# Optimization experiments

Measured on AMD Instinct MI355X. Metric: run time of the kernel, lower is better.

## Reference

```python
import jax, jax.numpy as jnp
import numpy as np

B, T = 4096, 512          # batch, max seq len
V, E, H, O = 57, 20, 128, 18  # vocab, embed, hidden, classes


def setup_inputs() -> dict:
    key = jax.random.key(0)
    ks = jax.random.split(key, 9)
    x = jax.random.randint(ks[0], (B, T), 0, V)
    lens = jax.random.randint(ks[1], (B,), 1, T + 1)
    x_lengths = jnp.sort(lens)[::-1]  # pack_padded_sequence needs descending lengths
    s = 1.0 / np.sqrt(H)
    emb = jax.random.normal(ks[2], (V, E), dtype=jnp.float32)
    W_ih = jax.random.uniform(ks[3], (H, E), minval=-s, maxval=s, dtype=jnp.float32)
    W_hh = jax.random.uniform(ks[4], (H, H), minval=-s, maxval=s, dtype=jnp.float32)
    b_ih = jax.random.uniform(ks[5], (H,), minval=-s, maxval=s, dtype=jnp.float32)
    b_hh = jax.random.uniform(ks[6], (H,), minval=-s, maxval=s, dtype=jnp.float32)
    so = 1.0 / np.sqrt(H)
    W_out = jax.random.uniform(ks[7], (O, H), minval=-so, maxval=so, dtype=jnp.float32)
    b_out = jax.random.uniform(ks[8], (O,), minval=-so, maxval=so, dtype=jnp.float32)
    return {"x": x, "x_lengths": x_lengths, "emb": emb, "W_ih": W_ih,
            "W_hh": W_hh, "b_ih": b_ih, "b_hh": b_hh, "W_out": W_out, "b_out": b_out}


def reference(x, x_lengths, emb, W_ih, W_hh, b_ih, b_hh, W_out, b_out):
    xe = emb[x]                                            # [B,T,E] embedding gather
    # precompute input projection + both biases once (hoisted out of recurrence)
    xw = jnp.einsum('bte,he->bth', xe, W_ih) + b_ih + b_hh  # [B,T,H]
    valid = jnp.arange(T)[None, :] < x_lengths[:, None]     # [B,T] packed-seq mask

    def step(h, inp):
        xw_t, v_t = inp                                     # [B,H], [B]
        h_new = jnp.tanh(xw_t + h @ W_hh.T)
        # packed RNN: stop updating once past this sequence's length,
        # so the final h equals the hidden state at step len-1
        h = jnp.where(v_t[:, None], h_new, h)
        return h, None

    h0 = jnp.zeros((B, H), dtype=xw.dtype)
    hT, _ = jax.lax.scan(step, h0, (jnp.swapaxes(xw, 0, 1), valid.T))  # scan over T
    logits = jax.nn.relu(hT) @ W_out.T + b_out              # [B,O]
    return jax.nn.log_softmax(logits, axis=1)
```

## Files before the change

### kernel.cpp

```cpp
#include <hip/hip_runtime.h>
#include <math.h>

#define Bn 4096
#define Tn 512
#define Vn 57
#define En 20
#define Hn 128
#define On 18
#define ROWS 16
#define NTHR 512
#define NBLK (Bn / ROWS)
#define XWSTR 132
#define XBSTR 516
#define HFSTR 132
#define ASCALE 2.8853900817779268f

typedef _Float16 half8  __attribute__((ext_vector_type(8)));
typedef __fp16   fp16x2 __attribute__((ext_vector_type(2)));
typedef float    floatx4 __attribute__((ext_vector_type(4)));

__device__ __forceinline__ float tanh_scaled(float z) {
    float e = __builtin_amdgcn_exp2f(z);
    float r = __builtin_amdgcn_rcpf(e + 1.0f);
    return fmaf(-2.0f, r, 1.0f);
}

__device__ __forceinline__ unsigned pk_u32(fp16x2 v) {
    union { fp16x2 h; unsigned u; } c; c.h = v; return c.u;
}

__launch_bounds__(NTHR, 2)
__global__ void rnn_mfma_kernel(const int* __restrict__ x,
                                const int* __restrict__ xlen,
                                const float* __restrict__ emb,
                                const float* __restrict__ W_ih,
                                const float* __restrict__ W_hh,
                                const float* __restrict__ b_ih,
                                const float* __restrict__ b_hh,
                                const float* __restrict__ W_out,
                                const float* __restrict__ b_out,
                                float* __restrict__ out)
{
    __shared__ __align__(16) uint4 exB[2][4][64];
    __shared__ __align__(16) float sXW[Vn * XWSTR];
    __shared__ __align__(16) float sHf[ROWS * HFSTR];
    __shared__ __align__(16) unsigned char sXb[ROWS * XBSTR];
    __shared__ float sLogit[ROWS][On];
    __shared__ float sMLS[ROWS];
    __shared__ float sPad[6200];

    const int tid  = threadIdx.x;
    const int blk  = blockIdx.x;
    const int row0 = blk * ROWS;

    ((volatile float*)sPad)[tid % 6200] = 0.0f;

    const int w    = tid >> 6;
    const int lane = tid & 63;
    const int n    = lane & 15;
    const int q    = lane >> 4;
    const int kcW  = w >> 1;
    const int bsel = w & 1;

    half8 Ah[4];
    const int f = 32 * kcW + 8 * (n >> 2) + 4 * bsel + (n & 3);
    #pragma unroll
    for (int kc = 0; kc < 4; ++kc) {
        const float* p = &W_hh[f * Hn + kc * 32 + q * 8];
        #pragma unroll
        for (int i = 0; i < 8; ++i)
            Ah[kc][i] = (_Float16)(p[i] * ASCALE);
    }

    for (int idx = tid; idx < Vn * Hn; idx += NTHR) {
        int vo = idx >> 7, ff = idx & 127;
        float acc = b_ih[ff] + b_hh[ff];
        #pragma unroll
        for (int e = 0; e < En; ++e)
            acc = fmaf(emb[vo * En + e], W_ih[ff * En + e], acc);
        sXW[vo * XWSTR + ff] = acc * ASCALE;
    }
    for (int idx = tid * 4; idx < ROWS * Tn; idx += NTHR * 4) {
        int4 v = *(const int4*)&x[row0 * Tn + idx];
        int r = idx >> 9, t = idx & 511;
        uchar4 bb;
        bb.x = (unsigned char)v.x; bb.y = (unsigned char)v.y;
        bb.z = (unsigned char)v.z; bb.w = (unsigned char)v.w;
        *(uchar4*)&sXb[r * XBSTR + t] = bb;
    }
    for (int idx = tid; idx < 2 * 4 * 64; idx += NTHR)
        ((uint4*)exB)[idx] = make_uint4(0u, 0u, 0u, 0u);
    __syncthreads();

    const int Lmax  = xlen[row0];
    const int len_n = xlen[row0 + n];
    const int wOffH = 32 * kcW + 8 * q + 4 * bsel;

    int    idN;
    float4 XWc;
    {
        int id0 = sXb[n * XBSTR];
        XWc = *(const float4*)&sXW[id0 * XWSTR + wOffH];
        idN = sXb[n * XBSTR + (Lmax > 1 ? 1 : 0)];
    }
    float hreg[4] = {0.f, 0.f, 0.f, 0.f};

    #define RNN_STEP(BR, BW, t)                                                   \
    {                                                                             \
        half8 bf0 = *(const half8*)&exB[BR][0][lane];                             \
        half8 bf1 = *(const half8*)&exB[BR][1][lane];                             \
        half8 bf2 = *(const half8*)&exB[BR][2][lane];                             \
        half8 bf3 = *(const half8*)&exB[BR][3][lane];                             \
        float4 XWn = *(const float4*)&sXW[idN * XWSTR + wOffH];                   \
        int tn = (t) + 2;                                                         \
        int idN2 = sXb[n * XBSTR + (tn < Lmax ? tn : Lmax - 1)];                  \
        floatx4 a0 = {XWc.x, XWc.y, XWc.z, XWc.w};                                \
        floatx4 a1 = {0.f, 0.f, 0.f, 0.f};                                        \
        floatx4 a2 = {0.f, 0.f, 0.f, 0.f};                                        \
        floatx4 a3 = {0.f, 0.f, 0.f, 0.f};                                        \
        a0 = __builtin_amdgcn_mfma_f32_16x16x32_f16(Ah[0], bf0, a0, 0, 0, 0);     \
        a1 = __builtin_amdgcn_mfma_f32_16x16x32_f16(Ah[1], bf1, a1, 0, 0, 0);     \
        a2 = __builtin_amdgcn_mfma_f32_16x16x32_f16(Ah[2], bf2, a2, 0, 0, 0);     \
        a3 = __builtin_amdgcn_mfma_f32_16x16x32_f16(Ah[3], bf3, a3, 0, 0, 0);     \
        const bool upd = ((t) < len_n);                                           \
        _Pragma("unroll")                                                         \
        for (int i = 0; i < 4; ++i) {                                             \
            float v = tanh_scaled((a0[i] + a1[i]) + (a2[i] + a3[i]));             \
            hreg[i] = upd ? v : hreg[i];                                          \
        }                                                                         \
        uint2 pk;                                                                 \
        pk.x = pk_u32(__builtin_amdgcn_cvt_pkrtz(hreg[0], hreg[1]));              \
        pk.y = pk_u32(__builtin_amdgcn_cvt_pkrtz(hreg[2], hreg[3]));              \
        *(uint2*)((_Float16*)&exB[BW][kcW][0] + lane * 8 + 4 * bsel) = pk;        \
        XWc = XWn; idN = idN2;                                                    \
        __syncthreads();                                                          \
    }

    int t = 0;
    for (; t + 2 <= Lmax; t += 2) {
        RNN_STEP(0, 1, t);
        RNN_STEP(1, 0, t + 1);
    }
    if (t < Lmax) {
        RNN_STEP(0, 1, t);
    }
    #undef RNN_STEP

    {
        float4 f0;
        f0.x = hreg[0]; f0.y = hreg[1]; f0.z = hreg[2]; f0.w = hreg[3];
        *(float4*)&sHf[n * HFSTR + wOffH] = f0;
    }
    __syncthreads();

    for (int it = tid; it < ROWS * On; it += NTHR) {
        int r = it / On, c = it % On;
        float acc = b_out[c];
        for (int k = 0; k < Hn; ++k) {
            float hv = sHf[r * HFSTR + k];
            hv = hv > 0.0f ? hv : 0.0f;
            acc = fmaf(hv, W_out[c * Hn + k], acc);
        }
        sLogit[r][c] = acc;
    }
    __syncthreads();

    if (tid < ROWS) {
        float m = -INFINITY;
        #pragma unroll
        for (int c = 0; c < On; ++c) m = fmaxf(m, sLogit[tid][c]);
        float s = 0.0f;
        #pragma unroll
        for (int c = 0; c < On; ++c) s += __expf(sLogit[tid][c] - m);
        sMLS[tid] = m + __logf(s);
    }
    __syncthreads();

    for (int it = tid; it < ROWS * On; it += NTHR) {
        int r = it / On, c = it % On;
        out[(row0 + r) * On + c] = sLogit[r][c] - sMLS[r];
    }
}

extern "C" void kernel_launch(void* const* d_in, const int* in_sizes, int n_in,
                              void* d_out, int out_size, void* d_ws, size_t ws_size,
                              hipStream_t stream) {
    const int*   x     = (const int*)d_in[0];
    const int*   xlen  = (const int*)d_in[1];
    const float* emb   = (const float*)d_in[2];
    const float* W_ih  = (const float*)d_in[3];
    const float* W_hh  = (const float*)d_in[4];
    const float* b_ih  = (const float*)d_in[5];
    const float* b_hh  = (const float*)d_in[6];
    const float* W_out = (const float*)d_in[7];
    const float* b_out = (const float*)d_in[8];
    float*       out   = (float*)d_out;

    rnn_mfma_kernel<<<NBLK, NTHR, 0, stream>>>(x, xlen, emb, W_ih, W_hh,
                                               b_ih, b_hh, W_out, b_out, out);
}
```

Before: 242.8 us.

## Run each RNN block as a single wavefront with register-resident hidden state

Each 16-row block now runs as one 64-thread wavefront that issues all 32 MFMAs per timestep, instead of 8 waves that exchange hidden-state fragments through LDS. The fp16 packing of hreg maps straight onto the next step's B operand in registers, so the per-step LDS round trip and __syncthreads barrier are gone. The input-projection table is rebuilt with per-thread W_ih rows held in registers, and the LDS padding that limited occupancy is removed. The cost is heavy register use (128 A-fragment registers, 32 hidden values, 8 XW prefetches) and a serial dependency chain per wave, so latency hiding now has to come from running many blocks per CU.

```diff
diff --git a/kernel.cpp b/kernel.cpp
--- a/kernel.cpp
+++ b/kernel.cpp
@@ -8,7 +8,7 @@
 #define Hn 128
 #define On 18
 #define ROWS 16
-#define NTHR 512
+#define NTHR 64
 #define NBLK (Bn / ROWS)
 #define XWSTR 132
 #define XBSTR 516
@@ -29,7 +29,11 @@
     union { fp16x2 h; unsigned u; } c; c.h = v; return c.u;
 }
 
-__launch_bounds__(NTHR, 2)
+__device__ __forceinline__ half8 as_half8(uint4 v) {
+    union { uint4 u; half8 h; } c; c.u = v; return c.h;
+}
+
+__launch_bounds__(NTHR, 1)
 __global__ void rnn_mfma_kernel(const int* __restrict__ x,
                                 const int* __restrict__ xlen,
                                 const float* __restrict__ emb,
@@ -41,44 +45,38 @@
                                 const float* __restrict__ b_out,
                                 float* __restrict__ out)
 {
-    __shared__ __align__(16) uint4 exB[2][4][64];
     __shared__ __align__(16) float sXW[Vn * XWSTR];
     __shared__ __align__(16) float sHf[ROWS * HFSTR];
     __shared__ __align__(16) unsigned char sXb[ROWS * XBSTR];
     __shared__ float sLogit[ROWS][On];
     __shared__ float sMLS[ROWS];
-    __shared__ float sPad[6200];
 
     const int tid  = threadIdx.x;
     const int blk  = blockIdx.x;
     const int row0 = blk * ROWS;
-
-    ((volatile float*)sPad)[tid % 6200] = 0.0f;
-
-    const int w    = tid >> 6;
-    const int lane = tid & 63;
-    const int n    = lane & 15;
-    const int q    = lane >> 4;
-    const int kcW  = w >> 1;
-    const int bsel = w & 1;
-
-    half8 Ah[4];
-    const int f = 32 * kcW + 8 * (n >> 2) + 4 * bsel + (n & 3);
-    #pragma unroll
-    for (int kc = 0; kc < 4; ++kc) {
-        const float* p = &W_hh[f * Hn + kc * 32 + q * 8];
-        #pragma unroll
-        for (int i = 0; i < 8; ++i)
-            Ah[kc][i] = (_Float16)(p[i] * ASCALE);
-    }
-
-    for (int idx = tid; idx < Vn * Hn; idx += NTHR) {
-        int vo = idx >> 7, ff = idx & 127;
-        float acc = b_ih[ff] + b_hh[ff];
-        #pragma unroll
-        for (int e = 0; e < En; ++e)
-            acc = fmaf(emb[vo * En + e], W_ih[ff * En + e], acc);
-        sXW[vo * XWSTR + ff] = acc * ASCALE;
+    const int n    = tid & 15;
+    const int q    = tid >> 4;
+
+    {
+        float wA[En], wB[En];
+        #pragma unroll
+        for (int e = 0; e < En; ++e) {
+            wA[e] = W_ih[tid * En + e];
+            wB[e] = W_ih[(tid + 64) * En + e];
+        }
+        const float bA = b_ih[tid] + b_hh[tid];
+        const float bB = b_ih[tid + 64] + b_hh[tid + 64];
+        for (int vo = 0; vo < Vn; ++vo) {
+            float aA = bA, aB = bB;
+            #pragma unroll
+            for (int e = 0; e < En; ++e) {
+                float ev = emb[vo * En + e];
+                aA = fmaf(ev, wA[e], aA);
+                aB = fmaf(ev, wB[e], aB);
+            }
+            sXW[vo * XWSTR + tid]      = aA * ASCALE;
+            sXW[vo * XWSTR + tid + 64] = aB * ASCALE;
+        }
     }
     for (int idx = tid * 4; idx < ROWS * Tn; idx += NTHR * 4) {
         int4 v = *(const int4*)&x[row0 * Tn + idx];
@@ -88,68 +86,102 @@
         bb.z = (unsigned char)v.z; bb.w = (unsigned char)v.w;
         *(uchar4*)&sXb[r * XBSTR + t] = bb;
     }
-    for (int idx = tid; idx < 2 * 4 * 64; idx += NTHR)
-        ((uint4*)exB)[idx] = make_uint4(0u, 0u, 0u, 0u);
+
+    half8 Ah[8][4];
+    #pragma unroll
+    for (int tau = 0; tau < 8; ++tau) {
+        const int f = 32 * (tau >> 1) + 8 * (n >> 2) + 4 * (tau & 1) + (n & 3);
+        #pragma unroll
+        for (int kc = 0; kc < 4; ++kc) {
+            const float* p = &W_hh[f * Hn + kc * 32 + q * 8];
+            #pragma unroll
+            for (int i = 0; i < 8; ++i)
+                Ah[tau][kc][i] = (_Float16)(p[i] * ASCALE);
+        }
+    }
     __syncthreads();
 
     const int Lmax  = xlen[row0];
     const int len_n = xlen[row0 + n];
-    const int wOffH = 32 * kcW + 8 * q + 4 * bsel;
-
+
+    float4 XWc[8];
     int    idN;
-    float4 XWc;
     {
         int id0 = sXb[n * XBSTR];
-        XWc = *(const float4*)&sXW[id0 * XWSTR + wOffH];
+        #pragma unroll
+        for (int tau = 0; tau < 8; ++tau)
+            XWc[tau] = *(const float4*)&sXW[id0 * XWSTR + 32 * (tau >> 1) + 8 * q + 4 * (tau & 1)];
         idN = sXb[n * XBSTR + (Lmax > 1 ? 1 : 0)];
     }
-    float hreg[4] = {0.f, 0.f, 0.f, 0.f};
-
-    #define RNN_STEP(BR, BW, t)                                                   \
+
+    float hreg[32];
+    #pragma unroll
+    for (int i = 0; i < 32; ++i) hreg[i] = 0.f;
+    uint4 bF[4];
+    #pragma unroll
+    for (int c = 0; c < 4; ++c) bF[c] = make_uint4(0u, 0u, 0u, 0u);
+
+    #define RNN_STEP(t)                                                           \
     {                                                                             \
-        half8 bf0 = *(const half8*)&exB[BR][0][lane];                             \
-        half8 bf1 = *(const half8*)&exB[BR][1][lane];                             \
-        half8 bf2 = *(const half8*)&exB[BR][2][lane];                             \
-        half8 bf3 = *(const half8*)&exB[BR][3][lane];                             \
-        float4 XWn = *(const float4*)&sXW[idN * XWSTR + wOffH];                   \
+        half8 b0 = as_half8(bF[0]), b1 = as_half8(bF[1]);                         \
+        half8 b2 = as_half8(bF[2]), b3 = as_half8(bF[3]);                         \
+        floatx4 a[8];                                                             \
+        _Pragma("unroll")                                                         \
+        for (int tau = 0; tau < 8; ++tau) {                                       \
+            floatx4 ci = {XWc[tau].x, XWc[tau].y, XWc[tau].z, XWc[tau].w};        \
+            a[tau] = __builtin_amdgcn_mfma_f32_16x16x32_f16(Ah[tau][0], b0, ci, 0, 0, 0); \
+        }                                                                         \
+        _Pragma("unroll")                                                         \
+        for (int tau = 0; tau < 8; ++tau)                                         \
+            XWc[tau] = *(const float4*)&sXW[idN * XWSTR + 32 * (tau >> 1) + 8 * q + 4 * (tau & 1)]; \
         int tn = (t) + 2;                                                         \
         int idN2 = sXb[n * XBSTR + (tn < Lmax ? tn : Lmax - 1)];                  \
-        floatx4 a0 = {XWc.x, XWc.y, XWc.z, XWc.w};                                \
-        floatx4 a1 = {0.f, 0.f, 0.f, 0.f};                                        \
-        floatx4 a2 = {0.f, 0.f, 0.f, 0.f};                                        \
-        floatx4 a3 = {0.f, 0.f, 0.f, 0.f};                                        \
-        a0 = __builtin_amdgcn_mfma_f32_16x16x32_f16(Ah[0], bf0, a0, 0, 0, 0);     \
-        a1 = __builtin_amdgcn_mfma_f32_16x16x32_f16(Ah[1], bf1, a1, 0, 0, 0);     \
-        a2 = __builtin_amdgcn_mfma_f32_16x16x32_f16(Ah[2], bf2, a2, 0, 0, 0);     \
-        a3 = __builtin_amdgcn_mfma_f32_16x16x32_f16(Ah[3], bf3, a3, 0, 0, 0);     \
+        _Pragma("unroll")                                                         \
+        for (int tau = 0; tau < 8; ++tau)                                         \
+            a[tau] = __builtin_amdgcn_mfma_f32_16x16x32_f16(Ah[tau][1], b1, a[tau], 0, 0, 0); \
+        _Pragma("unroll")                                                         \
+        for (int tau = 0; tau < 8; ++tau)                                         \
+            a[tau] = __builtin_amdgcn_mfma_f32_16x16x32_f16(Ah[tau][2], b2, a[tau], 0, 0, 0); \
+        _Pragma("unroll")                                                         \
+        for (int tau = 0; tau < 8; ++tau)                                         \
+            a[tau] = __builtin_amdgcn_mfma_f32_16x16x32_f16(Ah[tau][3], b3, a[tau], 0, 0, 0); \
         const bool upd = ((t) < len_n);                                           \
         _Pragma("unroll")                                                         \
-        for (int i = 0; i < 4; ++i) {                                             \
-            float v = tanh_scaled((a0[i] + a1[i]) + (a2[i] + a3[i]));             \
-            hreg[i] = upd ? v : hreg[i];                                          \
+        for (int tau = 0; tau < 8; ++tau) {                                       \
+            _Pragma("unroll")                                                     \
+            for (int i = 0; i < 4; ++i) {                                         \
+                float v = tanh_scaled(a[tau][i]);                                 \
+                hreg[4 * tau + i] = upd ? v : hreg[4 * tau + i];                  \
+            }                                                                     \
         }                                                                         \
-        uint2 pk;                                                                 \
-        pk.x = pk_u32(__builtin_amdgcn_cvt_pkrtz(hreg[0], hreg[1]));              \
-        pk.y = pk_u32(__builtin_amdgcn_cvt_pkrtz(hreg[2], hreg[3]));              \
-        *(uint2*)((_Float16*)&exB[BW][kcW][0] + lane * 8 + 4 * bsel) = pk;        \
-        XWc = XWn; idN = idN2;                                                    \
-        __syncthreads();                                                          \
+        _Pragma("unroll")                                                         \
+        for (int c = 0; c < 4; ++c) {                                             \
+            uint4 pk;                                                             \
+            pk.x = pk_u32(__builtin_amdgcn_cvt_pkrtz(hreg[8 * c + 0], hreg[8 * c + 1])); \
+            pk.y = pk_u32(__builtin_amdgcn_cvt_pkrtz(hreg[8 * c + 2], hreg[8 * c + 3])); \
+            pk.z = pk_u32(__builtin_amdgcn_cvt_pkrtz(hreg[8 * c + 4], hreg[8 * c + 5])); \
+            pk.w = pk_u32(__builtin_amdgcn_cvt_pkrtz(hreg[8 * c + 6], hreg[8 * c + 7])); \
+            bF[c] = pk;                                                           \
+        }                                                                         \
+        idN = idN2;                                                               \
     }
 
     int t = 0;
     for (; t + 2 <= Lmax; t += 2) {
-        RNN_STEP(0, 1, t);
-        RNN_STEP(1, 0, t + 1);
+        RNN_STEP(t);
+        RNN_STEP(t + 1);
     }
     if (t < Lmax) {
-        RNN_STEP(0, 1, t);
+        RNN_STEP(t);
     }
     #undef RNN_STEP
 
-    {
+    #pragma unroll
+    for (int tau = 0; tau < 8; ++tau) {
         float4 f0;
-        f0.x = hreg[0]; f0.y = hreg[1]; f0.z = hreg[2]; f0.w = hreg[3];
-        *(float4*)&sHf[n * HFSTR + wOffH] = f0;
+        f0.x = hreg[4 * tau + 0]; f0.y = hreg[4 * tau + 1];
+        f0.z = hreg[4 * tau + 2]; f0.w = hreg[4 * tau + 3];
+        *(float4*)&sHf[n * HFSTR + 32 * (tau >> 1) + 8 * q + 4 * (tau & 1)] = f0;
     }
     __syncthreads();
 
```

Result: slower. 460.6 us (+89.7%).
